# Performance work log

Hardware: AMD Instinct MI355X
Metric: run time of the kernel (lower is better)

Reference implementation:

```python
import jax, jax.numpy as jnp
import numpy as np

EMB = 768
HEADS = 12
HEAD_DIM = EMB // HEADS
SEQ = 4096
BATCH = 1


def setup_inputs() -> dict:
    key = jax.random.key(0)
    ks = jax.random.split(key, 9)
    s = 1.0 / np.sqrt(EMB)
    return {
        "x": jax.random.normal(ks[0], (BATCH, SEQ, EMB), dtype=jnp.float32),
        "wq": jax.random.normal(ks[1], (EMB, EMB), dtype=jnp.float32) * s,
        "bq": jax.random.normal(ks[2], (EMB,), dtype=jnp.float32) * s,
        "wk": jax.random.normal(ks[3], (EMB, EMB), dtype=jnp.float32) * s,
        "bk": jax.random.normal(ks[4], (EMB,), dtype=jnp.float32) * s,
        "wv": jax.random.normal(ks[5], (EMB, EMB), dtype=jnp.float32) * s,
        "bv": jax.random.normal(ks[6], (EMB,), dtype=jnp.float32) * s,
        "wo": jax.random.normal(ks[7], (EMB, EMB), dtype=jnp.float32) * s,
        "bo": jax.random.normal(ks[8], (EMB,), dtype=jnp.float32) * s,
    }


def reference(x, wq, bq, wk, bk, wv, bv, wo, bo):
    b, n, _ = x.shape
    # projections: [b, n, emb] -> [b, heads, n, head_dim]
    def split_heads(t):
        return t.reshape(b, n, HEADS, HEAD_DIM).transpose(0, 2, 1, 3)
    q = split_heads(x @ wq + bq)
    k = split_heads(x @ wk + bk)
    v = split_heads(x @ wv + bv)
    # full N x N scores (naive attention, as in the original)
    scores = jnp.einsum("bhqd,bhkd->bhqk", q, k)
    causal = jnp.triu(jnp.ones((n, n), dtype=bool), k=1)
    scores = jnp.where(causal, -jnp.inf, scores)
    weights = jax.nn.softmax(scores / np.sqrt(HEAD_DIM), axis=-1)
    # dropout with rate 0.0 is identity (eval mode)
    ctx = jnp.einsum("bhqk,bhkd->bhqd", weights, v)
    ctx = ctx.transpose(0, 2, 1, 3).reshape(b, n, EMB)
    return ctx @ wo + bo
```

## Files before the change

### kernel.cpp

```cpp
#include <hip/hip_runtime.h>
#include <stdint.h>

#define SEQ 4096
#define EMB 768
#define HEADS 12
#define HD 64

typedef __attribute__((ext_vector_type(8))) short short8;
typedef __attribute__((ext_vector_type(4))) short short4v;
typedef __attribute__((ext_vector_type(8))) __bf16 bf16x8;
typedef __attribute__((ext_vector_type(4))) __bf16 bf16x4;
typedef __attribute__((ext_vector_type(4))) float f32x4;

#define QSCALE 0.18033688011112043f

static __device__ __forceinline__ unsigned short f2bf(float f) {
    unsigned int u = __builtin_bit_cast(unsigned int, f);
    unsigned int r = 0x7fffu + ((u >> 16) & 1u);
    u += r;
    return (unsigned short)(u >> 16);
}

static __device__ __forceinline__ f32x4 mfma32(short8 a, short8 b, f32x4 c) {
    return __builtin_amdgcn_mfma_f32_16x16x32_bf16(
        __builtin_bit_cast(bf16x8, a), __builtin_bit_cast(bf16x8, b), c, 0, 0, 0);
}

static __device__ __forceinline__ f32x4 mfma16(short4v a, short4v b, f32x4 c) {
#if __has_builtin(__builtin_amdgcn_mfma_f32_16x16x16_bf16)
    return __builtin_amdgcn_mfma_f32_16x16x16_bf16(
        __builtin_bit_cast(bf16x4, a), __builtin_bit_cast(bf16x4, b), c, 0, 0, 0);
#else
    return __builtin_amdgcn_mfma_f32_16x16x16bf16_1k(a, b, c, 0, 0, 0);
#endif
}

static __device__ __forceinline__ short4v pack4bf(float a, float b, float c, float d) {
#if __has_builtin(__builtin_amdgcn_cvt_pk_bf16_f32)
    typedef __attribute__((ext_vector_type(2))) __bf16 bf16x2;
    bf16x2 lo = __builtin_amdgcn_cvt_pk_bf16_f32(a, b);
    bf16x2 hi = __builtin_amdgcn_cvt_pk_bf16_f32(c, d);
    uint2 u = {__builtin_bit_cast(unsigned int, lo), __builtin_bit_cast(unsigned int, hi)};
    return __builtin_bit_cast(short4v, u);
#else
    short4v p;
    p[0] = (short)f2bf(a); p[1] = (short)f2bf(b);
    p[2] = (short)f2bf(c); p[3] = (short)f2bf(d);
    return p;
#endif
}

static __device__ __forceinline__ void load_lds16(const void* g, void* l) {
    __builtin_amdgcn_global_load_lds(
        (const __attribute__((address_space(1))) unsigned int*)(uintptr_t)g,
        (__attribute__((address_space(3))) unsigned int*)(uintptr_t)l, 16, 0, 0);
}

static __device__ __forceinline__ int pid_of(int h, int i128, int ch) {
    int b = (i128 < 20) ? (i128 - 10)
                        : (i128 < 30 ? 10 + (i128 - 20) * 2 : 30 + (i128 - 30) * 3);
    return h * 36 + b + (ch - 1);
}

static __device__ __forceinline__ void softmax_step(f32x4* st, float& m_i, float& l_i,
                                                    f32x4* O, short4v* pk) {
    float mx = -3.0e38f;
    for (int nt = 0; nt < 4; nt++)
        for (int r = 0; r < 4; r++) mx = fmaxf(mx, st[nt][r]);
    mx = fmaxf(mx, __shfl_xor(mx, 16));
    mx = fmaxf(mx, __shfl_xor(mx, 32));
    const bool inc = mx > m_i;
    if (__ballot(inc)) {
        const float mn = inc ? mx : m_i;
        const float alpha = __builtin_amdgcn_exp2f(m_i - mn);
        m_i = mn;
        l_i *= alpha;
        for (int dt = 0; dt < 4; dt++)
            for (int r = 0; r < 4; r++) O[dt][r] *= alpha;
    }
    float rs = 0.f;
    for (int nt = 0; nt < 4; nt++) {
        float p0 = __builtin_amdgcn_exp2f(st[nt][0] - m_i);
        float p1 = __builtin_amdgcn_exp2f(st[nt][1] - m_i);
        float p2 = __builtin_amdgcn_exp2f(st[nt][2] - m_i);
        float p3 = __builtin_amdgcn_exp2f(st[nt][3] - m_i);
        rs += p0 + p1 + p2 + p3;
        pk[nt] = pack4bf(p0, p1, p2, p3);
    }
    rs += __shfl_xor(rs, 16);
    rs += __shfl_xor(rs, 32);
    l_i += rs;
}

__global__ __launch_bounds__(256) void convert_all(const float* __restrict__ x,
                                                   const float* __restrict__ wq,
                                                   const float* __restrict__ wk,
                                                   const float* __restrict__ wv,
                                                   const float* __restrict__ wo,
                                                   unsigned short* __restrict__ xb,
                                                   unsigned short* __restrict__ wqkvT,
                                                   unsigned short* __restrict__ woT) {
    __shared__ float Ls[64][65];
    const int bid = blockIdx.x;
    if (bid < 3072) {
        int i = bid * 256 + threadIdx.x;
        float4 v = ((const float4*)x)[i];
        ushort4 o = {f2bf(v.x), f2bf(v.y), f2bf(v.z), f2bf(v.w)};
        ((ushort4*)xb)[i] = o;
        return;
    }
    const int idx = bid - 3072;
    const int z = idx / 144;
    const int bx = (idx % 144) / 12, by = idx % 12;
    const float* W = (z == 0) ? wq : (z == 1) ? wk : (z == 2) ? wv : wo;
    unsigned short* dst = (z < 3) ? (wqkvT + (size_t)z * EMB * EMB) : woT;
    const int k0 = bx * 64, n0 = by * 64;
    const int r = threadIdx.x >> 2, c0 = (threadIdx.x & 3) * 16;
    for (int j = 0; j < 16; j += 4) {
        float4 v = *(const float4*)&W[(size_t)(k0 + r) * EMB + n0 + c0 + j];
        Ls[r][c0 + j] = v.x;
        Ls[r][c0 + j + 1] = v.y;
        Ls[r][c0 + j + 2] = v.z;
        Ls[r][c0 + j + 3] = v.w;
    }
    __syncthreads();
    unsigned short tmp[16];
    for (int j = 0; j < 16; j++) tmp[j] = f2bf(Ls[c0 + j][r]);
    *(uint4*)&dst[(size_t)(n0 + r) * EMB + k0 + c0] = *(uint4*)tmp;
    *(uint4*)&dst[(size_t)(n0 + r) * EMB + k0 + c0 + 8] = *(uint4*)(tmp + 8);
}

__global__ __launch_bounds__(256) void gemm_qkv(const unsigned short* __restrict__ A,
                                                const unsigned short* __restrict__ Bt,
                                                const float* __restrict__ b0p,
                                                const float* __restrict__ b1p,
                                                const float* __restrict__ b2p,
                                                unsigned short* __restrict__ QKb,
                                                unsigned short* __restrict__ Vtb) {
    __shared__ __align__(16) unsigned short SMEM[16384];
    const int tid = threadIdx.x;
    const int wave = tid >> 6, lane = tid & 63, quad = lane >> 4, l16 = lane & 15;
    const int m0 = blockIdx.x * 128, n0 = blockIdx.y * 128;
    const int wm = (wave >> 1) * 64, wn = (wave & 1) * 64;
    const int lrow = lane >> 2, lcol = (lane & 3) * 8;

    f32x4 acc[4][4] = {};

    for (int t = 0; t < 2; t++) {
        int row = wave * 32 + t * 16 + lrow;
        load_lds16(&A[(size_t)(m0 + row) * EMB + lcol], &SMEM[(wave * 2 + t) * 512]);
        load_lds16(&Bt[(size_t)(n0 + row) * EMB + lcol], &SMEM[4096 + (wave * 2 + t) * 512]);
    }
    int buf = 0;
    for (int k0 = 0; k0 < EMB; k0 += 32) {
        __syncthreads();
        if (k0 + 32 < EMB) {
            unsigned short* A_ = &SMEM[(buf ^ 1) * 8192];
            unsigned short* B_ = A_ + 4096;
            for (int t = 0; t < 2; t++) {
                int row = wave * 32 + t * 16 + lrow;
                load_lds16(&A[(size_t)(m0 + row) * EMB + k0 + 32 + lcol], &A_[(wave * 2 + t) * 512]);
                load_lds16(&Bt[(size_t)(n0 + row) * EMB + k0 + 32 + lcol], &B_[(wave * 2 + t) * 512]);
            }
        }
        const unsigned short* A_ = &SMEM[buf * 8192];
        const unsigned short* B_ = A_ + 4096;
        short8 a[4], b[4];
        for (int i = 0; i < 4; i++) a[i] = *(const short8*)&A_[(wm + i * 16 + l16) * 32 + quad * 8];
        for (int i = 0; i < 4; i++) b[i] = *(const short8*)&B_[(wn + i * 16 + l16) * 32 + quad * 8];
        for (int i = 0; i < 4; i++)
            for (int j = 0; j < 4; j++) acc[i][j] = mfma32(a[i], b[j], acc[i][j]);
        buf ^= 1;
    }

    const int z = n0 / EMB;
    if (z < 2) {
        const float* bias = z ? b1p : b0p;
        const float sc = z ? 1.0f : QSCALE;
        for (int i = 0; i < 4; i++)
            for (int j = 0; j < 4; j++) {
                int mbase = m0 + wm + i * 16 + quad * 4;
                int n = n0 + wn + j * 16 + l16;
                float bv = bias[n - z * EMB];
                for (int r = 0; r < 4; r++)
                    QKb[(size_t)(mbase + r) * 1536 + n] = f2bf((acc[i][j][r] + bv) * sc);
            }
    } else {
        const int nn = n0 + wn + l16 - 2 * EMB;
        for (int j = 0; j < 4; j++) {
            __syncthreads();
            const float bv = b2p[nn + j * 16];
            const int nloc = (wave & 1) * 16 + l16;
            for (int i = 0; i < 4; i++) {
                ushort4 pk;
                pk.x = f2bf(acc[i][j][0] + bv);
                pk.y = f2bf(acc[i][j][1] + bv);
                pk.z = f2bf(acc[i][j][2] + bv);
                pk.w = f2bf(acc[i][j][3] + bv);
                *(ushort4*)&SMEM[nloc * 136 + wm + i * 16 + quad * 4] = pk;
            }
            __syncthreads();
            const int nl = tid >> 3, c = tid & 7;
            const int ng = (nl >> 4) * 64 + j * 16 + (nl & 15) + n0 - 2 * EMB;
            const int hh = ng >> 6, dd = ng & 63;
            unsigned short* dst = &Vtb[(size_t)(hh * HD + dd) * SEQ + m0];
            *(uint4*)&dst[c * 8] = *(uint4*)&SMEM[nl * 136 + c * 8];
            *(uint4*)&dst[64 + c * 8] = *(uint4*)&SMEM[nl * 136 + 64 + c * 8];
        }
    }
}

__global__ __launch_bounds__(256) void gemm_out(const unsigned short* __restrict__ A,
                                                const unsigned short* __restrict__ Bt,
                                                const float* __restrict__ bias,
                                                float* __restrict__ outp) {
    __shared__ __align__(16) unsigned short SMEM[12288];
    const int tid = threadIdx.x;
    const int wave = tid >> 6, lane = tid & 63, quad = lane >> 4, l16 = lane & 15;
    const int m0 = blockIdx.x * 64, n0 = blockIdx.y * 128;
    const int wm = (wave >> 1) * 32, wn = (wave & 1) * 64;
    const int lrow = lane >> 2, lcol = (lane & 3) * 8;

    f32x4 acc[2][4] = {};

    load_lds16(&A[(size_t)(m0 + wave * 16 + lrow) * EMB + lcol], &SMEM[wave * 512]);
    for (int t = 0; t < 2; t++) {
        int row = wave * 32 + t * 16 + lrow;
        load_lds16(&Bt[(size_t)(n0 + row) * EMB + lcol], &SMEM[4096 + (wave * 2 + t) * 512]);
    }
    int buf = 0;
    for (int k0 = 0; k0 < EMB; k0 += 32) {
        __syncthreads();
        if (k0 + 32 < EMB) {
            unsigned short* A_ = &SMEM[(buf ^ 1) * 2048];
            unsigned short* B_ = &SMEM[4096 + (buf ^ 1) * 4096];
            load_lds16(&A[(size_t)(m0 + wave * 16 + lrow) * EMB + k0 + 32 + lcol], &A_[wave * 512]);
            for (int t = 0; t < 2; t++) {
                int row = wave * 32 + t * 16 + lrow;
                load_lds16(&Bt[(size_t)(n0 + row) * EMB + k0 + 32 + lcol], &B_[(wave * 2 + t) * 512]);
            }
        }
        const unsigned short* A_ = &SMEM[buf * 2048];
        const unsigned short* B_ = &SMEM[4096 + buf * 4096];
        short8 a[2], b[4];
        for (int i = 0; i < 2; i++) a[i] = *(const short8*)&A_[(wm + i * 16 + l16) * 32 + quad * 8];
        for (int j = 0; j < 4; j++) b[j] = *(const short8*)&B_[(wn + j * 16 + l16) * 32 + quad * 8];
        for (int i = 0; i < 2; i++)
            for (int j = 0; j < 4; j++) acc[i][j] = mfma32(a[i], b[j], acc[i][j]);
        buf ^= 1;
    }

    for (int i = 0; i < 2; i++)
        for (int j = 0; j < 4; j++) {
            int mbase = m0 + wm + i * 16 + quad * 4;
            int n = n0 + wn + j * 16 + l16;
            float bv = bias[n];
            for (int r = 0; r < 4; r++) outp[(size_t)(mbase + r) * EMB + n] = acc[i][j][r] + bv;
        }
}

__global__ __launch_bounds__(512) void attn_kernel(const unsigned short* __restrict__ QKb,
                                                   const unsigned short* __restrict__ Vtb,
                                                   unsigned short* __restrict__ ctxb,
                                                   unsigned short* __restrict__ Op,
                                                   float* __restrict__ mArr,
                                                   float* __restrict__ lArr) {
    __shared__ __align__(16) unsigned short Ks[2][64 * 64];
    __shared__ __align__(16) unsigned short Vs[2][64 * 64];

    const int bid = blockIdx.x;
    const int h = bid % HEADS;
    const int r2 = 67 - bid / HEADS;
    int i128, ch, nch;
    if (r2 < 10) {
        i128 = r2; ch = 0; nch = 1;
    } else if (r2 < 30) {
        int t = r2 - 10; i128 = 10 + (t >> 1); ch = t & 1; nch = 2;
    } else if (r2 < 60) {
        int t = r2 - 30; i128 = 20 + t / 3; ch = t % 3; nch = 3;
    } else {
        int t = r2 - 60; i128 = 30 + (t >> 2); ch = t & 3; nch = 4;
    }
    const int T = 2 * i128 + 2;
    const int kb = ch * T / nch;
    const int ke = (ch + 1) * T / nch - 1;
    const int qbase = i128 * 128;
    const int tid = threadIdx.x;
    const int wave = tid >> 6, lane = tid & 63, quad = lane >> 4, l16 = lane & 15;

    const unsigned short* Qg = QKb + (size_t)h * HD;
    const unsigned short* Kg = QKb + (size_t)(EMB + h * HD);
    const unsigned short* Vh = Vtb + (size_t)h * HD * SEQ;

    const int q = qbase + wave * 16 + l16;
    const short8 bQ0 = *(const short8*)&Qg[(size_t)q * 1536 + quad * 8];
    const short8 bQ1 = *(const short8*)&Qg[(size_t)q * 1536 + 32 + quad * 8];

    const int srow = wave * 8 + ((lane >> 3));
    const int sg = (lane & 7) ^ (srow & 7);

    f32x4 O[4] = {};
    float m_i = -3.0e38f, l_i = 0.f;

    {
        const int kb64 = kb * 64;
        load_lds16(&Kg[(size_t)(kb64 + srow) * 1536 + sg * 8], &Ks[0][wave * 512]);
        load_lds16(&Vh[(size_t)srow * SEQ + kb64 + sg * 8], &Vs[0][wave * 512]);
    }
    int buf = 0;
    for (int kt = kb; kt <= ke; kt++) {
        const int kbase = kt * 64;
        __syncthreads();
        if (kt < ke) {
            const int nb = kbase + 64;
            load_lds16(&Kg[(size_t)(nb + srow) * 1536 + sg * 8], &Ks[buf ^ 1][wave * 512]);
            load_lds16(&Vh[(size_t)srow * SEQ + nb + sg * 8], &Vs[buf ^ 1][wave * 512]);
        }
        if (kbase <= qbase + wave * 16 + 15) {
            const int swr = l16 & 7;
            f32x4 st[4];
            for (int nt = 0; nt < 4; nt++) {
                short8 aK0 = *(const short8*)&Ks[buf][(nt * 16 + l16) * 64 + (quad ^ swr) * 8];
                short8 aK1 =
                    *(const short8*)&Ks[buf][(nt * 16 + l16) * 64 + ((quad + 4) ^ swr) * 8];
                f32x4 z = {};
                z = mfma32(aK0, bQ0, z);
                z = mfma32(aK1, bQ1, z);
                st[nt] = z;
            }
            if (kbase + 63 > qbase + wave * 16) {
                for (int nt = 0; nt < 4; nt++)
                    for (int r = 0; r < 4; r++)
                        if (kbase + nt * 16 + quad * 4 + r > q) st[nt][r] = -INFINITY;
            }

            short4v pk[4];
            softmax_step(st, m_i, l_i, O, pk);

            for (int dt = 0; dt < 4; dt++)
                for (int nt = 0; nt < 4; nt++) {
                    const int j = 4 * nt + quad;
                    short4v av = *(const short4v*)&Vs[buf][(dt * 16 + l16) * 64 +
                                                          (2 * ((j >> 1) ^ swr) + (j & 1)) * 4];
                    O[dt] = mfma16(av, pk[nt], O[dt]);
                }
        }
        buf ^= 1;
    }

    const int ql = wave * 16 + l16;
    if (nch == 1) {
        const float inv = 1.f / l_i;
        for (int dt = 0; dt < 4; dt++) {
            ushort4 o;
            o.x = f2bf(O[dt][0] * inv);
            o.y = f2bf(O[dt][1] * inv);
            o.z = f2bf(O[dt][2] * inv);
            o.w = f2bf(O[dt][3] * inv);
            *(ushort4*)&ctxb[(size_t)q * EMB + h * HD + dt * 16 + quad * 4] = o;
        }
    } else {
        if (ch == 0) {
            for (int dt = 0; dt < 4; dt++) {
                ushort4 o;
                o.x = f2bf(O[dt][0]);
                o.y = f2bf(O[dt][1]);
                o.z = f2bf(O[dt][2]);
                o.w = f2bf(O[dt][3]);
                *(ushort4*)&ctxb[(size_t)q * EMB + h * HD + dt * 16 + quad * 4] = o;
            }
        } else {
            const int pid = pid_of(h, i128, ch);
            for (int dt = 0; dt < 4; dt++) {
                ushort4 o;
                o.x = f2bf(O[dt][0]);
                o.y = f2bf(O[dt][1]);
                o.z = f2bf(O[dt][2]);
                o.w = f2bf(O[dt][3]);
                *(ushort4*)&Op[(size_t)pid * 8192 + ql * 64 + dt * 16 + quad * 4] = o;
            }
        }
        if (quad == 0) {
            const int mli = ((h * 32 + i128) * 4 + ch) * 128 + ql;
            mArr[mli] = m_i;
            lArr[mli] = l_i;
        }
    }
}

__global__ __launch_bounds__(256) void merge_kernel(const unsigned short* __restrict__ Op,
                                                    const float* __restrict__ mArr,
                                                    const float* __restrict__ lArr,
                                                    unsigned short* __restrict__ ctxb) {
    const int gid = blockIdx.x;
    const int h = gid % HEADS;
    const int i128 = 10 + gid / HEADS;
    const int nch = (i128 < 20) ? 2 : (i128 < 30) ? 3 : 4;
    const int q = threadIdx.x >> 1, d0 = (threadIdx.x & 1) * 32;
    const int mlbase = (h * 32 + i128) * 4;

    float mc[4], lc[4];
    for (int c = 0; c < nch; c++) {
        mc[c] = mArr[(mlbase + c) * 128 + q];
        lc[c] = lArr[(mlbase + c) * 128 + q];
    }
    float M = mc[0];
    for (int c = 1; c < nch; c++) M = fmaxf(M, mc[c]);
    float w[4], L = 0.f;
    for (int c = 0; c < nch; c++) {
        w[c] = __builtin_amdgcn_exp2f(mc[c] - M);
        L += w[c] * lc[c];
    }
    const float inv = 1.f / L;
    for (int c = 0; c < nch; c++) w[c] *= inv;

    unsigned short* dst = &ctxb[(size_t)(i128 * 128 + q) * EMB + h * HD + d0];
    for (int jj = 0; jj < 32; jj += 8) {
        uint4 u0 = *(const uint4*)&dst[jj];
        float f[8];
        const unsigned short* p0 = (const unsigned short*)&u0;
        for (int t = 0; t < 8; t++)
            f[t] = w[0] * __builtin_bit_cast(float, (unsigned int)p0[t] << 16);
        for (int c = 1; c < nch; c++) {
            const int pid = pid_of(h, i128, c);
            uint4 u = *(const uint4*)&Op[(size_t)pid * 8192 + q * 64 + d0 + jj];
            const unsigned short* p = (const unsigned short*)&u;
            for (int t = 0; t < 8; t++)
                f[t] += w[c] * __builtin_bit_cast(float, (unsigned int)p[t] << 16);
        }
        unsigned short o[8];
        for (int t = 0; t < 8; t++) o[t] = f2bf(f[t]);
        *(uint4*)&dst[jj] = *(uint4*)o;
    }
}

extern "C" void kernel_launch(void* const* d_in, const int* in_sizes, int n_in,
                              void* d_out, int out_size, void* d_ws, size_t ws_size,
                              hipStream_t stream) {
    const float* x = (const float*)d_in[0];
    const float* wq = (const float*)d_in[1];
    const float* bq = (const float*)d_in[2];
    const float* wk = (const float*)d_in[3];
    const float* bk = (const float*)d_in[4];
    const float* wv = (const float*)d_in[5];
    const float* bv = (const float*)d_in[6];
    const float* wo = (const float*)d_in[7];
    const float* bo = (const float*)d_in[8];

    unsigned short* ws = (unsigned short*)d_ws;
    unsigned short* xb = ws;
    unsigned short* wqkvT = xb + SEQ * EMB;
    unsigned short* woT = wqkvT + 3 * EMB * EMB;
    unsigned short* QKb = woT + EMB * EMB;
    unsigned short* Vtb = QKb + (size_t)SEQ * 1536;
    unsigned short* ctxb = Vtb + HEADS * SEQ * HD;
    unsigned short* Op = xb;
    float* mArr = (float*)(ws + 3538944);
    float* lArr = mArr + 196608;

    convert_all<<<dim3(3072 + 576), 256, 0, stream>>>(x, wq, wk, wv, wo, xb, wqkvT, woT);
    gemm_qkv<<<dim3(SEQ / 128, 3 * EMB / 128), 256, 0, stream>>>(
        xb, wqkvT, bq, bk, bv, QKb, Vtb);
    attn_kernel<<<dim3(12 * 68), 512, 0, stream>>>(QKb, Vtb, ctxb, Op, mArr, lArr);
    merge_kernel<<<dim3(264), 256, 0, stream>>>(Op, mArr, lArr, ctxb);
    gemm_out<<<dim3(SEQ / 64, EMB / 128), 256, 0, stream>>>(ctxb, woT, bo, (float*)d_out);
}
```

Measured before the change: 194.8 us.

## Replace direct-to-LDS double buffering with register-staged single-buffer K/V loads

The attention kernel drops the double-buffered LDS tiles loaded through global-to-LDS instructions. It now prefetches the next K/V tile into registers, writes the current tile to a single LDS buffer between two barriers, and uses a new XOR swizzle for V reads. The aim is to halve LDS use, which may allow more blocks per CU, and to apply a swizzle that avoids bank conflicts on V. In exchange it adds a second barrier per iteration plus extra VGPRs and LDS store instructions, and fully masked waves now only skip the compute after those barriers.

```diff
diff --git a/kernel.cpp b/kernel.cpp
--- a/kernel.cpp
+++ b/kernel.cpp
@@ -265,8 +265,8 @@
                                                    unsigned short* __restrict__ Op,
                                                    float* __restrict__ mArr,
                                                    float* __restrict__ lArr) {
-    __shared__ __align__(16) unsigned short Ks[2][64 * 64];
-    __shared__ __align__(16) unsigned short Vs[2][64 * 64];
+    __shared__ __align__(16) unsigned short Ks[64 * 64];
+    __shared__ __align__(16) unsigned short Vs[64 * 64];
 
     const int bid = blockIdx.x;
     const int h = bid % HEADS;
@@ -296,56 +296,59 @@
     const short8 bQ0 = *(const short8*)&Qg[(size_t)q * 1536 + quad * 8];
     const short8 bQ1 = *(const short8*)&Qg[(size_t)q * 1536 + 32 + quad * 8];
 
-    const int srow = wave * 8 + ((lane >> 3));
-    const int sg = (lane & 7) ^ (srow & 7);
+    const int row = tid >> 3, t8 = tid & 7;
+    const int swk = row & 7, swv = row & 15;
 
     f32x4 O[4] = {};
     float m_i = -3.0e38f, l_i = 0.f;
 
+    uint4 kr, vr;
     {
         const int kb64 = kb * 64;
-        load_lds16(&Kg[(size_t)(kb64 + srow) * 1536 + sg * 8], &Ks[0][wave * 512]);
-        load_lds16(&Vh[(size_t)srow * SEQ + kb64 + sg * 8], &Vs[0][wave * 512]);
-    }
-    int buf = 0;
+        kr = *(const uint4*)&Kg[(size_t)(kb64 + row) * 1536 + t8 * 8];
+        vr = *(const uint4*)&Vh[(size_t)row * SEQ + kb64 + t8 * 8];
+    }
+
     for (int kt = kb; kt <= ke; kt++) {
         const int kbase = kt * 64;
         __syncthreads();
+        *(uint4*)&Ks[row * 64 + (t8 ^ swk) * 8] = kr;
+        *(uint2*)&Vs[row * 64 + ((2 * t8) ^ swv) * 4] = ((const uint2*)&vr)[0];
+        *(uint2*)&Vs[row * 64 + ((2 * t8 + 1) ^ swv) * 4] = ((const uint2*)&vr)[1];
         if (kt < ke) {
             const int nb = kbase + 64;
-            load_lds16(&Kg[(size_t)(nb + srow) * 1536 + sg * 8], &Ks[buf ^ 1][wave * 512]);
-            load_lds16(&Vh[(size_t)srow * SEQ + nb + sg * 8], &Vs[buf ^ 1][wave * 512]);
-        }
-        if (kbase <= qbase + wave * 16 + 15) {
-            const int swr = l16 & 7;
-            f32x4 st[4];
+            kr = *(const uint4*)&Kg[(size_t)(nb + row) * 1536 + t8 * 8];
+            vr = *(const uint4*)&Vh[(size_t)row * SEQ + nb + t8 * 8];
+        }
+        __syncthreads();
+
+        if (kbase > qbase + wave * 16 + 15) continue;
+
+        const int swr = l16 & 7;
+        f32x4 st[4];
+        for (int nt = 0; nt < 4; nt++) {
+            short8 aK0 = *(const short8*)&Ks[(nt * 16 + l16) * 64 + (quad ^ swr) * 8];
+            short8 aK1 = *(const short8*)&Ks[(nt * 16 + l16) * 64 + ((quad + 4) ^ swr) * 8];
+            f32x4 z = {};
+            z = mfma32(aK0, bQ0, z);
+            z = mfma32(aK1, bQ1, z);
+            st[nt] = z;
+        }
+        if (kbase + 63 > qbase + wave * 16) {
+            for (int nt = 0; nt < 4; nt++)
+                for (int r = 0; r < 4; r++)
+                    if (kbase + nt * 16 + quad * 4 + r > q) st[nt][r] = -INFINITY;
+        }
+
+        short4v pk[4];
+        softmax_step(st, m_i, l_i, O, pk);
+
+        for (int dt = 0; dt < 4; dt++)
             for (int nt = 0; nt < 4; nt++) {
-                short8 aK0 = *(const short8*)&Ks[buf][(nt * 16 + l16) * 64 + (quad ^ swr) * 8];
-                short8 aK1 =
-                    *(const short8*)&Ks[buf][(nt * 16 + l16) * 64 + ((quad + 4) ^ swr) * 8];
-                f32x4 z = {};
-                z = mfma32(aK0, bQ0, z);
-                z = mfma32(aK1, bQ1, z);
-                st[nt] = z;
-            }
-            if (kbase + 63 > qbase + wave * 16) {
-                for (int nt = 0; nt < 4; nt++)
-                    for (int r = 0; r < 4; r++)
-                        if (kbase + nt * 16 + quad * 4 + r > q) st[nt][r] = -INFINITY;
-            }
-
-            short4v pk[4];
-            softmax_step(st, m_i, l_i, O, pk);
-
-            for (int dt = 0; dt < 4; dt++)
-                for (int nt = 0; nt < 4; nt++) {
-                    const int j = 4 * nt + quad;
-                    short4v av = *(const short4v*)&Vs[buf][(dt * 16 + l16) * 64 +
-                                                          (2 * ((j >> 1) ^ swr) + (j & 1)) * 4];
-                    O[dt] = mfma16(av, pk[nt], O[dt]);
-                }
-        }
-        buf ^= 1;
+                short4v av =
+                    *(const short4v*)&Vs[(dt * 16 + l16) * 64 + ((4 * nt + quad) ^ l16) * 4];
+                O[dt] = mfma16(av, pk[nt], O[dt]);
+            }
     }
 
     const int ql = wave * 16 + l16;
```

Result: faster. 186.4 us (-4.3%).
